# Kernel tuning notes

Hardware: AMD Instinct MI355X
Metric: run time of the kernel (lower is better)

## Reference

```python
import jax, jax.numpy as jnp
import numpy as np

NUM_RELATIONS = 3


def _rgcn(x, W_rel, W_root, bias, src, dst, etype):
    # PyG RGCNConv: out = x @ W_root + bias + sum_r mean_{e: type(e)=r, dst(e)=i} (x_src @ W_r)
    n = x.shape[0]
    xr = jnp.einsum('ni,rio->rno', x, W_rel)          # [R, N, F] relation-transformed nodes
    msg = xr[etype, src]                               # [E, F] per-edge messages
    out = x @ W_root + bias
    for r in range(NUM_RELATIONS):
        m = (etype == r)
        s = jax.ops.segment_sum(jnp.where(m[:, None], msg, 0.0), dst, num_segments=n)
        c = jax.ops.segment_sum(m.astype(x.dtype), dst, num_segments=n)
        out = out + s / jnp.maximum(c, 1.0)[:, None]   # mean aggregation per relation
    return out


def _gate(h, q, Wg, bg, Wq, bq):
    # h: [BN, F], q: [B, L, F]
    B, L, F = q.shape
    N = h.shape[0] // B
    h3 = h.reshape(B, N, F)
    # w_gate(cat([h_i, q_l])) = h_i @ Wg[:, :F].T + q_l @ Wg[:, F:].T + bg
    hg = jnp.einsum('bnf,gf->bng', h3, Wg[:, :F])                    # [B,N,F]
    qg = jnp.einsum('blf,gf->blg', q, Wg[:, F:]) + bg                # [B,L,F]
    attn = jax.nn.sigmoid(hg[:, :, None, :] + qg[:, None, :, :])     # [B,N,L,F]
    qi = jnp.einsum('bnlf,blf->bnf', attn, q)                        # [B,N,F]
    alpha = jax.nn.sigmoid(
        jnp.einsum('bnf,gf->bng', h3, Wq[:, :F])
        + jnp.einsum('bnf,gf->bng', qi, Wq[:, F:]) + bq)
    hn = alpha * jnp.tanh(qi) + (1.0 - alpha) * h3
    return hn.reshape(B * N, F)


def setup_inputs() -> dict:
    key = jax.random.key(0)
    ks = jax.random.split(key, 16)
    F = 768
    BN, E, B, L = 2048, 65536, 8, 64
    s = 0.02
    return {
        'x': jax.random.normal(ks[0], (BN, F), jnp.float32),
        'edge_index': jax.random.randint(ks[1], (2, E), 0, BN),
        'edge_type': jax.random.randint(ks[2], (E,), 0, NUM_RELATIONS),
        'query_embs': jax.random.normal(ks[3], (B, L, F), jnp.float32),
        'W_rel1': jax.random.normal(ks[4], (NUM_RELATIONS, F, F), jnp.float32) * s,
        'W_root1': jax.random.normal(ks[5], (F, F), jnp.float32) * s,
        'b1': jnp.zeros((F,), jnp.float32),
        'W_rel2': jax.random.normal(ks[6], (NUM_RELATIONS, F, F), jnp.float32) * s,
        'W_root2': jax.random.normal(ks[7], (F, F), jnp.float32) * s,
        'b2': jnp.zeros((F,), jnp.float32),
        'Wg': jax.random.normal(ks[8], (F, 2 * F), jnp.float32) * s,
        'bg': jnp.zeros((F,), jnp.float32),
        'Wq': jax.random.normal(ks[9], (F, 2 * F), jnp.float32) * s,
        'bq': jnp.zeros((F,), jnp.float32),
    }


def reference(x, edge_index, edge_type, query_embs,
              W_rel1, W_root1, b1, W_rel2, W_root2, b2, Wg, bg, Wq, bq):
    src, dst = edge_index[0], edge_index[1]
    h = jax.nn.relu(_rgcn(x, W_rel1, W_root1, b1, src, dst, edge_type))
    h = _gate(h, query_embs, Wg, bg, Wq, bq)
    h = jax.nn.relu(_rgcn(h, W_rel2, W_root2, b2, src, dst, edge_type))
    h = _gate(h, query_embs, Wg, bg, Wq, bq)
    return h
```

## Files before the change

kernel.cpp:

```cpp
#include <hip/hip_runtime.h>
#include <hip/hip_bf16.h>
#include <cstdint>
#include <cstddef>

#define F 768

typedef float f32x4 __attribute__((ext_vector_type(4)));
typedef short s16x8 __attribute__((ext_vector_type(8)));
typedef short s16x4 __attribute__((ext_vector_type(4)));

#define NEG_LOG2E (-1.4426950408889634f)

__device__ __forceinline__ float bf2f(unsigned short u) {
  union { unsigned int i; float f; } v; v.i = ((unsigned int)u) << 16; return v.f;
}
__device__ __forceinline__ unsigned short f2bf(float f) {
  union { float f; unsigned int i; } v; v.f = f;
  unsigned int r = v.i + 0x7FFF + ((v.i >> 16) & 1);
  return (unsigned short)(r >> 16);
}

#if __has_builtin(__builtin_amdgcn_exp2f)
__device__ __forceinline__ float fexp2(float x) { return __builtin_amdgcn_exp2f(x); }
#else
__device__ __forceinline__ float fexp2(float x) { return exp2f(x); }
#endif
#if __has_builtin(__builtin_amdgcn_rcpf)
__device__ __forceinline__ float frcp(float x) { return __builtin_amdgcn_rcpf(x); }
#else
__device__ __forceinline__ float frcp(float x) { return 1.0f / x; }
#endif

__device__ __forceinline__ float ftanh(float x) {
  float t = fexp2(x * 2.8853900817779268f);
  float s = frcp(t + 1.0f);
  return fmaf(-2.0f, s, 1.0f);
}

__device__ __forceinline__ void gload16(const void* g, void* l) {
  __builtin_amdgcn_global_load_lds(
      (const __attribute__((address_space(1))) void*)g,
      (__attribute__((address_space(3))) void*)l, 16, 0, 0);
}

__global__ void khist(const int* __restrict__ ei, int E, int* __restrict__ cnt) {
  int e = blockIdx.x * blockDim.x + threadIdx.x;
  if (e < E) atomicAdd(&cnt[ei[E + e]], 1);
}

__global__ void kscan(const int* __restrict__ cnt, int* __restrict__ offs, int n) {
  __shared__ int part[256];
  int t = threadIdx.x;
  const int per = n / 256;
  int local[8];
  int s = 0;
  for (int j = 0; j < per; ++j) { local[j] = cnt[t * per + j]; s += local[j]; }
  part[t] = s;
  __syncthreads();
  for (int d = 1; d < 256; d <<= 1) {
    int v = (t >= d) ? part[t - d] : 0;
    __syncthreads();
    part[t] += v;
    __syncthreads();
  }
  int run = (t == 0) ? 0 : part[t - 1];
  for (int j = 0; j < per; ++j) { offs[t * per + j] = run; run += local[j]; }
  if (t == 255) offs[n] = run;
}

__global__ void kscatter(const int* __restrict__ ei, const int* __restrict__ et, int E,
                         const int* __restrict__ offs, int* __restrict__ cur,
                         int* __restrict__ sorted) {
  int e = blockIdx.x * blockDim.x + threadIdx.x;
  if (e >= E) return;
  int dst = ei[E + e];
  int pos = offs[dst] + atomicAdd(&cur[dst], 1);
  sorted[pos] = ei[e] | (et[e] << 16);
}

__global__ void kcvt(const float* __restrict__ src, int lds_,
                     unsigned short* __restrict__ dst, int ldd) {
  const int r = blockIdx.x, c = threadIdx.x * 4;
  float4 v = *(const float4*)(src + (size_t)r * lds_ + c);
  s16x4 o;
  o[0] = (short)f2bf(v.x); o[1] = (short)f2bf(v.y);
  o[2] = (short)f2bf(v.z); o[3] = (short)f2bf(v.w);
  *(s16x4*)(dst + (size_t)r * ldd + c) = o;
}

__global__ void kcvtw(const float* __restrict__ Wg, const float* __restrict__ Wq,
                      unsigned short* __restrict__ Wgq, unsigned short* __restrict__ WgR,
                      unsigned short* __restrict__ WqR) {
  const int b = blockIdx.x, c = threadIdx.x * 4;
  const float* srow;
  unsigned short* drow;
  int off;
  if (b < 1536) {
    srow = (b < 768) ? Wg + (size_t)b * 1536 : Wq + (size_t)(b - 768) * 1536;
    drow = Wgq + (size_t)b * 768;
    off = 0;
  } else if (b < 2304) {
    srow = Wg + (size_t)(b - 1536) * 1536;
    drow = WgR + (size_t)(b - 1536) * 768;
    off = 768;
  } else {
    srow = Wq + (size_t)(b - 2304) * 1536;
    drow = WqR + (size_t)(b - 2304) * 768;
    off = 768;
  }
  float4 v = *(const float4*)(srow + off + c);
  s16x4 o;
  o[0] = (short)f2bf(v.x); o[1] = (short)f2bf(v.y);
  o[2] = (short)f2bf(v.z); o[3] = (short)f2bf(v.w);
  *(s16x4*)(drow + c) = o;
}

__global__ void ktrans(const float* __restrict__ Wr1, const float* __restrict__ Wl1,
                       const float* __restrict__ Wr2, const float* __restrict__ Wl2,
                       unsigned short* __restrict__ Wcat1, unsigned short* __restrict__ Wcat2) {
  __shared__ float tile[64][65];
  const int z = blockIdx.z, layer = z >> 2, part = z & 3;
  const float* src = (part == 0) ? (layer ? Wr2 : Wr1)
                                 : ((layer ? Wl2 : Wl1) + (size_t)(part - 1) * F * F);
  unsigned short* dst = (layer ? Wcat2 : Wcat1) + part * F;
  const int kt = blockIdx.x * 64, nt = blockIdx.y * 64;
  const int t = threadIdx.x, c = t & 63, r4 = t >> 6;
#pragma unroll
  for (int it = 0; it < 16; ++it) {
    int kk = r4 + it * 4;
    tile[kk][c] = src[(size_t)(kt + kk) * F + nt + c];
  }
  __syncthreads();
#pragma unroll
  for (int it = 0; it < 16; ++it) {
    int rr = r4 + it * 4;
    dst[(size_t)(nt + rr) * 3072 + kt + c] = f2bf(tile[c][rr]);
  }
}

__global__ void kagg(const int* __restrict__ offs, const int* __restrict__ sorted,
                     const unsigned short* __restrict__ hin,
                     unsigned short* __restrict__ dst) {
  const int i = blockIdx.x, t = threadIdx.x;
  const int col = t * 4;
  float a0[4] = {}, a1[4] = {}, a2[4] = {};
  int c0 = 0, c1 = 0, c2 = 0;
  const int beg = offs[i], end = offs[i + 1];
  int e = beg;
  for (; e + 1 < end; e += 2) {
    int p0 = sorted[e], p1 = sorted[e + 1];
    s16x4 w0 = *(const s16x4*)(hin + (size_t)(p0 & 0xFFFF) * 3072 + col);
    s16x4 w1 = *(const s16x4*)(hin + (size_t)(p1 & 0xFFFF) * 3072 + col);
    int r0 = p0 >> 16, r1 = p1 >> 16;
    float v0[4], v1[4];
#pragma unroll
    for (int j = 0; j < 4; ++j) {
      v0[j] = bf2f((unsigned short)w0[j]);
      v1[j] = bf2f((unsigned short)w1[j]);
    }
    if (r0 == 0)      { c0++; for (int j = 0; j < 4; ++j) a0[j] += v0[j]; }
    else if (r0 == 1) { c1++; for (int j = 0; j < 4; ++j) a1[j] += v0[j]; }
    else              { c2++; for (int j = 0; j < 4; ++j) a2[j] += v0[j]; }
    if (r1 == 0)      { c0++; for (int j = 0; j < 4; ++j) a0[j] += v1[j]; }
    else if (r1 == 1) { c1++; for (int j = 0; j < 4; ++j) a1[j] += v1[j]; }
    else              { c2++; for (int j = 0; j < 4; ++j) a2[j] += v1[j]; }
  }
  if (e < end) {
    int p0 = sorted[e];
    s16x4 w0 = *(const s16x4*)(hin + (size_t)(p0 & 0xFFFF) * 3072 + col);
    int r0 = p0 >> 16;
    float v0[4];
#pragma unroll
    for (int j = 0; j < 4; ++j) v0[j] = bf2f((unsigned short)w0[j]);
    if (r0 == 0)      { c0++; for (int j = 0; j < 4; ++j) a0[j] += v0[j]; }
    else if (r0 == 1) { c1++; for (int j = 0; j < 4; ++j) a1[j] += v0[j]; }
    else              { c2++; for (int j = 0; j < 4; ++j) a2[j] += v0[j]; }
  }
  const float i0 = frcp((float)(c0 > 0 ? c0 : 1));
  const float i1 = frcp((float)(c1 > 0 ? c1 : 1));
  const float i2 = frcp((float)(c2 > 0 ? c2 : 1));
  unsigned short* d = dst + (size_t)i * 3072 + col;
  s16x4 o;
#pragma unroll
  for (int j = 0; j < 4; ++j) o[j] = (short)f2bf(a0[j] * i0);
  *(s16x4*)d = o;
#pragma unroll
  for (int j = 0; j < 4; ++j) o[j] = (short)f2bf(a1[j] * i1);
  *(s16x4*)(d + F) = o;
#pragma unroll
  for (int j = 0; j < 4; ++j) o[j] = (short)f2bf(a2[j] * i2);
  *(s16x4*)(d + 2 * F) = o;
}

template <int EPI>
__launch_bounds__(256)
__global__ void kmm(const unsigned short* __restrict__ A, int lda,
                    const unsigned short* __restrict__ B, int ldb,
                    float* __restrict__ C, int ldc, int K,
                    const float* __restrict__ bias,
                    const float* __restrict__ aux1,
                    const unsigned short* __restrict__ aux2,
                    unsigned short* __restrict__ C2, int ldc2, float escale) {
  __shared__ unsigned short Asb[2][64 * 64];
  __shared__ unsigned short Bsb[2][64 * 64];
  const int t = threadIdx.x;
  const int lane = t & 63, wid = t >> 6;
  const int wr = wid >> 1, wc = wid & 1;
  const int bm = blockIdx.x * 64, bn = blockIdx.y * 64;

  const int srow = lane >> 3, schunk = lane & 7;
  const int kxor = ((schunk ^ srow) << 3);
  const int rowA = wid * 16 + srow;
  const unsigned short* Ap = A + (size_t)(bm + rowA) * lda + kxor;
  const unsigned short* Bp = B + (size_t)(bn + rowA) * ldb + kxor;
  const int lbase = wid * 16 * 64;

  const int rA0 = wr * 32 + (lane & 15);
  const int rB0 = wc * 32 + (lane & 15);
  const int l7 = lane & 7, lq = lane >> 4;
  const int s8_0 = (((0 * 4 + lq) ^ l7) << 3);
  const int s8_1 = (((1 * 4 + lq) ^ l7) << 3);

  f32x4 acc[2][2] = {};

  auto stage = [&](int cb, int k0) {
#pragma unroll
    for (int j = 0; j < 2; ++j) {
      gload16(Ap + (size_t)j * 8 * lda + k0, &Asb[cb][lbase + j * 512]);
      gload16(Bp + (size_t)j * 8 * ldb + k0, &Bsb[cb][lbase + j * 512]);
    }
  };

  stage(0, 0);
  __syncthreads();
  int cur = 0;
  for (int k0 = 0; k0 < K; k0 += 64) {
    if (k0 + 64 < K) stage(cur ^ 1, k0 + 64);
    const unsigned short* As = Asb[cur];
    const unsigned short* Bs = Bsb[cur];
#pragma unroll
    for (int ks = 0; ks < 2; ++ks) {
      const int s8 = ks ? s8_1 : s8_0;
      s16x8 af[2], bf[2];
#pragma unroll
      for (int i = 0; i < 2; ++i)
        af[i] = *(const s16x8*)(As + (rA0 + i * 16) * 64 + s8);
#pragma unroll
      for (int n = 0; n < 2; ++n)
        bf[n] = *(const s16x8*)(Bs + (rB0 + n * 16) * 64 + s8);
#pragma unroll
      for (int i = 0; i < 2; ++i)
#pragma unroll
        for (int n = 0; n < 2; ++n)
          acc[i][n] = __builtin_amdgcn_mfma_f32_16x16x32_bf16(af[i], bf[n], acc[i][n], 0, 0, 0);
    }
    __syncthreads();
    cur ^= 1;
  }

#pragma unroll
  for (int i = 0; i < 2; ++i)
#pragma unroll
    for (int n = 0; n < 2; ++n)
#pragma unroll
      for (int j = 0; j < 4; ++j) {
        const int row = bm + wr * 32 + i * 16 + (lane >> 4) * 4 + j;
        const int col = bn + wc * 32 + n * 16 + (lane & 15);
        float v = acc[i][n][j];
        if (EPI == 3 || EPI == 4) {
          float zh = aux1[(size_t)row * 1536 + 768 + col];
          float z = v + bias[col] + zh;
          float al = frcp(1.0f + fexp2(z * NEG_LOG2E));
          float tq = aux1[(size_t)row * 1536 + col];
          float hv = bf2f(aux2[(size_t)row * 768 + col]);
          float o = al * tq + (1.0f - al) * hv;
          if (EPI == 3) C2[(size_t)row * ldc2 + col] = f2bf(o);
          else          C[(size_t)row * ldc + col] = o;
        } else if (EPI == 5) {
          float es = (bn < 768) ? escale : 1.0f;
          C[(size_t)row * ldc + col] = v * es;
        } else if (EPI == 6) {
          C[(size_t)row * ldc + col] = (v + bias[col]) * escale;
        }
      }
}

__launch_bounds__(256)
__global__ void kmm_pk(const unsigned short* __restrict__ A, int lda,
                       const unsigned short* __restrict__ B, int ldb,
                       float* __restrict__ P, int Ksplit, int pstride) {
  __shared__ unsigned short Asb[2][64 * 64];
  __shared__ unsigned short Bsb[2][64 * 64];
  const int t = threadIdx.x;
  const int lane = t & 63, wid = t >> 6;
  const int wr = wid >> 1, wc = wid & 1;
  const int bm = blockIdx.x * 64, bn = blockIdx.y * 64;
  const int kbase = blockIdx.z * Ksplit;
  float* Cp = P + (size_t)blockIdx.z * pstride;

  const int srow = lane >> 3, schunk = lane & 7;
  const int kxor = ((schunk ^ srow) << 3);
  const int rowA = wid * 16 + srow;
  const unsigned short* Ap = A + (size_t)(bm + rowA) * lda + kxor + kbase;
  const unsigned short* Bp = B + (size_t)(bn + rowA) * ldb + kxor + kbase;
  const int lbase = wid * 16 * 64;

  const int rA0 = wr * 32 + (lane & 15);
  const int rB0 = wc * 32 + (lane & 15);
  const int l7 = lane & 7, lq = lane >> 4;
  const int s8_0 = (((0 * 4 + lq) ^ l7) << 3);
  const int s8_1 = (((1 * 4 + lq) ^ l7) << 3);

  f32x4 acc[2][2] = {};

  auto stage = [&](int cb, int k0) {
#pragma unroll
    for (int j = 0; j < 2; ++j) {
      gload16(Ap + (size_t)j * 8 * lda + k0, &Asb[cb][lbase + j * 512]);
      gload16(Bp + (size_t)j * 8 * ldb + k0, &Bsb[cb][lbase + j * 512]);
    }
  };

  stage(0, 0);
  __syncthreads();
  int cur = 0;
  for (int k0 = 0; k0 < Ksplit; k0 += 64) {
    if (k0 + 64 < Ksplit) stage(cur ^ 1, k0 + 64);
    const unsigned short* As = Asb[cur];
    const unsigned short* Bs = Bsb[cur];
#pragma unroll
    for (int ks = 0; ks < 2; ++ks) {
      const int s8 = ks ? s8_1 : s8_0;
      s16x8 af[2], bf[2];
#pragma unroll
      for (int i = 0; i < 2; ++i)
        af[i] = *(const s16x8*)(As + (rA0 + i * 16) * 64 + s8);
#pragma unroll
      for (int n = 0; n < 2; ++n)
        bf[n] = *(const s16x8*)(Bs + (rB0 + n * 16) * 64 + s8);
#pragma unroll
      for (int i = 0; i < 2; ++i)
#pragma unroll
        for (int n = 0; n < 2; ++n)
          acc[i][n] = __builtin_amdgcn_mfma_f32_16x16x32_bf16(af[i], bf[n], acc[i][n], 0, 0, 0);
    }
    __syncthreads();
    cur ^= 1;
  }

#pragma unroll
  for (int i = 0; i < 2; ++i)
#pragma unroll
    for (int n = 0; n < 2; ++n)
#pragma unroll
      for (int j = 0; j < 4; ++j) {
        const int row = bm + wr * 32 + i * 16 + (lane >> 4) * 4 + j;
        const int col = bn + wc * 32 + n * 16 + (lane & 15);
        Cp[(size_t)row * F + col] = acc[i][n][j];
      }
}

__global__ void kep_relu(const float* __restrict__ P, int pstride,
                         const float* __restrict__ bias,
                         unsigned short* __restrict__ hb) {
  const int idx = (blockIdx.x * 256 + threadIdx.x) * 4;
  const int col = idx - (idx / F) * F;
  float4 s = *(const float4*)(P + idx);
  const float4 s1 = *(const float4*)(P + pstride + idx);
  const float4 s2 = *(const float4*)(P + 2 * (size_t)pstride + idx);
  const float4 s3 = *(const float4*)(P + 3 * (size_t)pstride + idx);
  const float4 bv = *(const float4*)(bias + col);
  s.x = fmaxf(s.x + s1.x + s2.x + s3.x + bv.x, 0.0f);
  s.y = fmaxf(s.y + s1.y + s2.y + s3.y + bv.y, 0.0f);
  s.z = fmaxf(s.z + s1.z + s2.z + s3.z + bv.z, 0.0f);
  s.w = fmaxf(s.w + s1.w + s2.w + s3.w + bv.w, 0.0f);
  s16x4 o;
  o[0] = (short)f2bf(s.x); o[1] = (short)f2bf(s.y);
  o[2] = (short)f2bf(s.z); o[3] = (short)f2bf(s.w);
  *(s16x4*)(hb + idx) = o;
}

__global__ void kqi(float* __restrict__ hgz, const float* __restrict__ q,
                    const float* __restrict__ qgp,
                    unsigned short* __restrict__ qib,
                    int npb, int L) {
  const int t = threadIdx.x;
  const int g0 = blockIdx.x * 2;
  const int b = g0 / npb;
  float hgv[2][3], acc[2][3];
#pragma unroll
  for (int nn = 0; nn < 2; ++nn)
#pragma unroll
    for (int c = 0; c < 3; ++c) {
      hgv[nn][c] = hgz[(size_t)(g0 + nn) * 1536 + c * 256 + t];
      acc[nn][c] = 0.0f;
    }
  const float* qb = q + (size_t)b * L * F;
  const float* qgb = qgp + (size_t)b * L * F;
#pragma unroll 4
  for (int l = 0; l < L; ++l) {
    float qr[3], qgr[3];
#pragma unroll
    for (int c = 0; c < 3; ++c) {
      qr[c] = qb[(size_t)l * F + c * 256 + t];
      qgr[c] = qgb[(size_t)l * F + c * 256 + t];
    }
#pragma unroll
    for (int nn = 0; nn < 2; ++nn)
#pragma unroll
      for (int c = 0; c < 3; ++c) {
        float s = frcp(1.0f + fexp2(hgv[nn][c] + qgr[c]));
        acc[nn][c] = fmaf(s, qr[c], acc[nn][c]);
      }
  }
#pragma unroll
  for (int nn = 0; nn < 2; ++nn)
#pragma unroll
    for (int c = 0; c < 3; ++c) {
      const int g = g0 + nn, cc = c * 256 + t;
      qib[(size_t)g * F + cc] = f2bf(acc[nn][c]);
      hgz[(size_t)g * 1536 + cc] = ftanh(acc[nn][c]);
    }
}

extern "C" void kernel_launch(void* const* d_in, const int* in_sizes, int n_in,
                              void* d_out, int out_size, void* d_ws, size_t ws_size,
                              hipStream_t stream) {
  const float* x = (const float*)d_in[0];
  const int* ei = (const int*)d_in[1];
  const int* et = (const int*)d_in[2];
  const float* q = (const float*)d_in[3];
  const float* Wrel1 = (const float*)d_in[4];
  const float* Wroot1 = (const float*)d_in[5];
  const float* b1 = (const float*)d_in[6];
  const float* Wrel2 = (const float*)d_in[7];
  const float* Wroot2 = (const float*)d_in[8];
  const float* b2 = (const float*)d_in[9];
  const float* Wg = (const float*)d_in[10];
  const float* bg = (const float*)d_in[11];
  const float* Wq = (const float*)d_in[12];
  const float* bq = (const float*)d_in[13];

  const int BNn = in_sizes[0] / F;
  const int E = in_sizes[1] / 2;
  const int L = 64;
  const int Bq = in_sizes[3] / (L * F);
  const int npb = BNn / Bq;
  const int ML = Bq * L;
  const int PSTR = BNn * F;
  float* out = (float*)d_out;

  char* p = (char*)d_ws;
  auto alloc = [&](size_t bytes) {
    void* r = (void*)p;
    p += (bytes + 255) & ~(size_t)255;
    return r;
  };
  int* cnt = (int*)alloc((size_t)BNn * 4);
  int* cur = (int*)alloc((size_t)BNn * 4);
  int* offs = (int*)alloc((size_t)(BNn + 1) * 4);
  int* sorted = (int*)alloc((size_t)E * 4);
  unsigned short* Acat = (unsigned short*)alloc((size_t)BNn * 3072 * 2);
  unsigned short* Wcat1 = (unsigned short*)alloc((size_t)F * 3072 * 2);
  unsigned short* Wcat2 = (unsigned short*)alloc((size_t)F * 3072 * 2);
  unsigned short* Wgq = (unsigned short*)alloc((size_t)1536 * F * 2);
  unsigned short* WgR = (unsigned short*)alloc((size_t)F * F * 2);
  unsigned short* WqR = (unsigned short*)alloc((size_t)F * F * 2);
  unsigned short* qbf = (unsigned short*)alloc((size_t)ML * F * 2);
  float* qg = (float*)alloc((size_t)ML * F * 4);
  unsigned short* hb = (unsigned short*)alloc((size_t)BNn * F * 2);
  float* hgz = (float*)alloc((size_t)BNn * 1536 * 4);
  unsigned short* qib = (unsigned short*)alloc((size_t)BNn * F * 2);
  float* parts = (float*)alloc((size_t)4 * PSTR * 4);

  hipMemsetAsync(cnt, 0, (size_t)BNn * 4, stream);
  hipMemsetAsync(cur, 0, (size_t)BNn * 4, stream);
  khist<<<(E + 255) / 256, 256, 0, stream>>>(ei, E, cnt);
  kscan<<<1, 256, 0, stream>>>(cnt, offs, BNn);
  kscatter<<<(E + 255) / 256, 256, 0, stream>>>(ei, et, E, offs, cur, sorted);

  kcvt<<<BNn, 192, 0, stream>>>(x, F, Acat, 3072);
  kcvt<<<ML, 192, 0, stream>>>(q, F, qbf, F);
  kcvtw<<<3072, 192, 0, stream>>>(Wg, Wq, Wgq, WgR, WqR);
  ktrans<<<dim3(12, 12, 8), 256, 0, stream>>>(Wroot1, Wrel1, Wroot2, Wrel2, Wcat1, Wcat2);

  kmm<6><<<dim3(ML / 64, F / 64), 256, 0, stream>>>(
      qbf, F, WgR, F, qg, F, F, bg, nullptr, nullptr, nullptr, 0, NEG_LOG2E);

  for (int layer = 0; layer < 2; ++layer) {
    const unsigned short* Wcat = layer ? Wcat2 : Wcat1;
    const float* bb = layer ? b2 : b1;

    kagg<<<BNn, 192, 0, stream>>>(offs, sorted, Acat, Acat + F);

    kmm_pk<<<dim3(BNn / 64, F / 64, 4), 256, 0, stream>>>(
        Acat, 3072, Wcat, 3072, parts, F, PSTR);

    kep_relu<<<(BNn * F) / 1024, 256, 0, stream>>>(parts, PSTR, bb, hb);

    kmm<5><<<dim3(BNn / 64, 1536 / 64), 256, 0, stream>>>(
        hb, F, Wgq, F, hgz, 1536, F, nullptr, nullptr, nullptr, nullptr, 0, NEG_LOG2E);

    kqi<<<BNn / 2, 256, 0, stream>>>(hgz, q, qg, qib, npb, L);

    if (layer == 0) {
      kmm<3><<<dim3(BNn / 64, F / 64), 256, 0, stream>>>(
          qib, F, WqR, F, nullptr, 0, F, bq, hgz, hb, Acat, 3072, 0.f);
    } else {
      kmm<4><<<dim3(BNn / 64, F / 64), 256, 0, stream>>>(
          qib, F, WqR, F, out, F, F, bq, hgz, hb, nullptr, 0, 0.f);
    }
  }
}
```

Before: 338.1 us.

## Fuse gate attention reduction into GEMM epilogue and merge small launches

Removes the separate kqi kernel by computing the sigmoid-weighted sum over query tokens in a new GEMM epilogue (EPI 7). It works directly on the accumulator tiles for the first 768 output columns, which avoids writing and rereading the hg half of hgz. It also merges the two conversion launches and the two memsets into one each, and unrolls the edge aggregation loop by four to issue more gathers in flight. The cost is that the epilogue does 64 iterations of exp and reciprocal per element inside the GEMM blocks, which can add register pressure and load imbalance because only half the column blocks do this work.

After: 335.0 us. About the same (-0.9%).

```diff
diff --git a/kernel.cpp b/kernel.cpp
--- a/kernel.cpp
+++ b/kernel.cpp
@@ -78,14 +78,18 @@
   sorted[pos] = ei[e] | (et[e] << 16);
 }
 
-__global__ void kcvt(const float* __restrict__ src, int lds_,
-                     unsigned short* __restrict__ dst, int ldd) {
+__global__ void kcvt(const float* __restrict__ x, const float* __restrict__ q, int nx,
+                     unsigned short* __restrict__ Acat, unsigned short* __restrict__ qbf) {
   const int r = blockIdx.x, c = threadIdx.x * 4;
-  float4 v = *(const float4*)(src + (size_t)r * lds_ + c);
+  const float* srow;
+  unsigned short* drow;
+  if (r < nx) { srow = x + (size_t)r * F; drow = Acat + (size_t)r * 3072; }
+  else        { srow = q + (size_t)(r - nx) * F; drow = qbf + (size_t)(r - nx) * F; }
+  float4 v = *(const float4*)(srow + c);
   s16x4 o;
   o[0] = (short)f2bf(v.x); o[1] = (short)f2bf(v.y);
   o[2] = (short)f2bf(v.z); o[3] = (short)f2bf(v.w);
-  *(s16x4*)(dst + (size_t)r * ldd + c) = o;
+  *(s16x4*)(drow + c) = o;
 }
 
 __global__ void kcvtw(const float* __restrict__ Wg, const float* __restrict__ Wq,
@@ -147,25 +151,26 @@
   int c0 = 0, c1 = 0, c2 = 0;
   const int beg = offs[i], end = offs[i + 1];
   int e = beg;
-  for (; e + 1 < end; e += 2) {
-    int p0 = sorted[e], p1 = sorted[e + 1];
-    s16x4 w0 = *(const s16x4*)(hin + (size_t)(p0 & 0xFFFF) * 3072 + col);
-    s16x4 w1 = *(const s16x4*)(hin + (size_t)(p1 & 0xFFFF) * 3072 + col);
-    int r0 = p0 >> 16, r1 = p1 >> 16;
-    float v0[4], v1[4];
-#pragma unroll
-    for (int j = 0; j < 4; ++j) {
-      v0[j] = bf2f((unsigned short)w0[j]);
-      v1[j] = bf2f((unsigned short)w1[j]);
-    }
-    if (r0 == 0)      { c0++; for (int j = 0; j < 4; ++j) a0[j] += v0[j]; }
-    else if (r0 == 1) { c1++; for (int j = 0; j < 4; ++j) a1[j] += v0[j]; }
-    else              { c2++; for (int j = 0; j < 4; ++j) a2[j] += v0[j]; }
-    if (r1 == 0)      { c0++; for (int j = 0; j < 4; ++j) a0[j] += v1[j]; }
-    else if (r1 == 1) { c1++; for (int j = 0; j < 4; ++j) a1[j] += v1[j]; }
-    else              { c2++; for (int j = 0; j < 4; ++j) a2[j] += v1[j]; }
-  }
-  if (e < end) {
+  for (; e + 3 < end; e += 4) {
+    int pk[4];
+#pragma unroll
+    for (int u = 0; u < 4; ++u) pk[u] = sorted[e + u];
+    s16x4 w[4];
+#pragma unroll
+    for (int u = 0; u < 4; ++u)
+      w[u] = *(const s16x4*)(hin + (size_t)(pk[u] & 0xFFFF) * 3072 + col);
+#pragma unroll
+    for (int u = 0; u < 4; ++u) {
+      int r = pk[u] >> 16;
+      float v[4];
+#pragma unroll
+      for (int j = 0; j < 4; ++j) v[j] = bf2f((unsigned short)w[u][j]);
+      if (r == 0)      { c0++; for (int j = 0; j < 4; ++j) a0[j] += v[j]; }
+      else if (r == 1) { c1++; for (int j = 0; j < 4; ++j) a1[j] += v[j]; }
+      else             { c2++; for (int j = 0; j < 4; ++j) a2[j] += v[j]; }
+    }
+  }
+  for (; e < end; ++e) {
     int p0 = sorted[e];
     s16x4 w0 = *(const s16x4*)(hin + (size_t)(p0 & 0xFFFF) * 3072 + col);
     int r0 = p0 >> 16;
@@ -200,7 +205,8 @@
                     const float* __restrict__ bias,
                     const float* __restrict__ aux1,
                     const unsigned short* __restrict__ aux2,
-                    unsigned short* __restrict__ C2, int ldc2, float escale) {
+                    unsigned short* __restrict__ C2, int ldc2,
+                    float escale, int Lq) {
   __shared__ unsigned short Asb[2][64 * 64];
   __shared__ unsigned short Bsb[2][64 * 64];
   const int t = threadIdx.x;
@@ -256,6 +262,49 @@
     }
     __syncthreads();
     cur ^= 1;
+  }
+
+  if (EPI == 7 && bn < 768) {
+    float hgp[2][2][4], qacc[2][2][4];
+#pragma unroll
+    for (int i = 0; i < 2; ++i)
+#pragma unroll
+      for (int n = 0; n < 2; ++n)
+#pragma unroll
+        for (int j = 0; j < 4; ++j) {
+          hgp[i][n][j] = acc[i][n][j] * NEG_LOG2E;
+          qacc[i][n][j] = 0.0f;
+        }
+    const int b = bm >> 8;
+    const int col0 = bn + wc * 32 + (lane & 15);
+    const float* qb = aux1 + (size_t)b * Lq * F;
+    const float* qgb = bias + (size_t)b * Lq * F;
+#pragma unroll 2
+    for (int l = 0; l < Lq; ++l) {
+      const float qg0 = qgb[(size_t)l * F + col0];
+      const float qg1 = qgb[(size_t)l * F + col0 + 16];
+      const float q0 = qb[(size_t)l * F + col0];
+      const float q1 = qb[(size_t)l * F + col0 + 16];
+#pragma unroll
+      for (int i = 0; i < 2; ++i)
+#pragma unroll
+        for (int j = 0; j < 4; ++j) {
+          qacc[i][0][j] = fmaf(frcp(1.0f + fexp2(hgp[i][0][j] + qg0)), q0, qacc[i][0][j]);
+          qacc[i][1][j] = fmaf(frcp(1.0f + fexp2(hgp[i][1][j] + qg1)), q1, qacc[i][1][j]);
+        }
+    }
+#pragma unroll
+    for (int i = 0; i < 2; ++i)
+#pragma unroll
+      for (int n = 0; n < 2; ++n)
+#pragma unroll
+        for (int j = 0; j < 4; ++j) {
+          const int row = bm + wr * 32 + i * 16 + (lane >> 4) * 4 + j;
+          const int col = col0 + n * 16;
+          C2[(size_t)row * 768 + col] = f2bf(qacc[i][n][j]);
+          C[(size_t)row * 1536 + col] = ftanh(qacc[i][n][j]);
+        }
+    return;
   }
 
 #pragma unroll
@@ -276,11 +325,10 @@
           float o = al * tq + (1.0f - al) * hv;
           if (EPI == 3) C2[(size_t)row * ldc2 + col] = f2bf(o);
           else          C[(size_t)row * ldc + col] = o;
-        } else if (EPI == 5) {
-          float es = (bn < 768) ? escale : 1.0f;
-          C[(size_t)row * ldc + col] = v * es;
         } else if (EPI == 6) {
           C[(size_t)row * ldc + col] = (v + bias[col]) * escale;
+        } else {
+          C[(size_t)row * ldc + col] = v;
         }
       }
 }
@@ -380,49 +428,6 @@
   *(s16x4*)(hb + idx) = o;
 }
 
-__global__ void kqi(float* __restrict__ hgz, const float* __restrict__ q,
-                    const float* __restrict__ qgp,
-                    unsigned short* __restrict__ qib,
-                    int npb, int L) {
-  const int t = threadIdx.x;
-  const int g0 = blockIdx.x * 2;
-  const int b = g0 / npb;
-  float hgv[2][3], acc[2][3];
-#pragma unroll
-  for (int nn = 0; nn < 2; ++nn)
-#pragma unroll
-    for (int c = 0; c < 3; ++c) {
-      hgv[nn][c] = hgz[(size_t)(g0 + nn) * 1536 + c * 256 + t];
-      acc[nn][c] = 0.0f;
-    }
-  const float* qb = q + (size_t)b * L * F;
-  const float* qgb = qgp + (size_t)b * L * F;
-#pragma unroll 4
-  for (int l = 0; l < L; ++l) {
-    float qr[3], qgr[3];
-#pragma unroll
-    for (int c = 0; c < 3; ++c) {
-      qr[c] = qb[(size_t)l * F + c * 256 + t];
-      qgr[c] = qgb[(size_t)l * F + c * 256 + t];
-    }
-#pragma unroll
-    for (int nn = 0; nn < 2; ++nn)
-#pragma unroll
-      for (int c = 0; c < 3; ++c) {
-        float s = frcp(1.0f + fexp2(hgv[nn][c] + qgr[c]));
-        acc[nn][c] = fmaf(s, qr[c], acc[nn][c]);
-      }
-  }
-#pragma unroll
-  for (int nn = 0; nn < 2; ++nn)
-#pragma unroll
-    for (int c = 0; c < 3; ++c) {
-      const int g = g0 + nn, cc = c * 256 + t;
-      qib[(size_t)g * F + cc] = f2bf(acc[nn][c]);
-      hgz[(size_t)g * 1536 + cc] = ftanh(acc[nn][c]);
-    }
-}
-
 extern "C" void kernel_launch(void* const* d_in, const int* in_sizes, int n_in,
                               void* d_out, int out_size, void* d_ws, size_t ws_size,
                               hipStream_t stream) {
@@ -445,7 +450,6 @@
   const int E = in_sizes[1] / 2;
   const int L = 64;
   const int Bq = in_sizes[3] / (L * F);
-  const int npb = BNn / Bq;
   const int ML = Bq * L;
   const int PSTR = BNn * F;
   float* out = (float*)d_out;
@@ -456,8 +460,9 @@
     p += (bytes + 255) & ~(size_t)255;
     return r;
   };
-  int* cnt = (int*)alloc((size_t)BNn * 4);
-  int* cur = (int*)alloc((size_t)BNn * 4);
+  int* cntcur = (int*)alloc((size_t)2 * BNn * 4);
+  int* cnt = cntcur;
+  int* cur = cntcur + BNn;
   int* offs = (int*)alloc((size_t)(BNn + 1) * 4);
   int* sorted = (int*)alloc((size_t)E * 4);
   unsigned short* Acat = (unsigned short*)alloc((size_t)BNn * 3072 * 2);
@@ -473,19 +478,17 @@
   unsigned short* qib = (unsigned short*)alloc((size_t)BNn * F * 2);
   float* parts = (float*)alloc((size_t)4 * PSTR * 4);
 
-  hipMemsetAsync(cnt, 0, (size_t)BNn * 4, stream);
-  hipMemsetAsync(cur, 0, (size_t)BNn * 4, stream);
+  hipMemsetAsync(cntcur, 0, (size_t)2 * BNn * 4, stream);
   khist<<<(E + 255) / 256, 256, 0, stream>>>(ei, E, cnt);
   kscan<<<1, 256, 0, stream>>>(cnt, offs, BNn);
   kscatter<<<(E + 255) / 256, 256, 0, stream>>>(ei, et, E, offs, cur, sorted);
 
-  kcvt<<<BNn, 192, 0, stream>>>(x, F, Acat, 3072);
-  kcvt<<<ML, 192, 0, stream>>>(q, F, qbf, F);
+  kcvt<<<BNn + ML, 192, 0, stream>>>(x, q, BNn, Acat, qbf);
   kcvtw<<<3072, 192, 0, stream>>>(Wg, Wq, Wgq, WgR, WqR);
   ktrans<<<dim3(12, 12, 8), 256, 0, stream>>>(Wroot1, Wrel1, Wroot2, Wrel2, Wcat1, Wcat2);
 
   kmm<6><<<dim3(ML / 64, F / 64), 256, 0, stream>>>(
-      qbf, F, WgR, F, qg, F, F, bg, nullptr, nullptr, nullptr, 0, NEG_LOG2E);
+      qbf, F, WgR, F, qg, F, F, bg, nullptr, nullptr, nullptr, 0, NEG_LOG2E, L);
 
   for (int layer = 0; layer < 2; ++layer) {
     const unsigned short* Wcat = layer ? Wcat2 : Wcat1;
@@ -498,17 +501,15 @@
 
     kep_relu<<<(BNn * F) / 1024, 256, 0, stream>>>(parts, PSTR, bb, hb);
 
-    kmm<5><<<dim3(BNn / 64, 1536 / 64), 256, 0, stream>>>(
-        hb, F, Wgq, F, hgz, 1536, F, nullptr, nullptr, nullptr, nullptr, 0, NEG_LOG2E);
-
-    kqi<<<BNn / 2, 256, 0, stream>>>(hgz, q, qg, qib, npb, L);
+    kmm<7><<<dim3(BNn / 64, 1536 / 64), 256, 0, stream>>>(
+        hb, F, Wgq, F, hgz, 1536, F, qg, q, nullptr, qib, F, 0.f, L);
 
     if (layer == 0) {
       kmm<3><<<dim3(BNn / 64, F / 64), 256, 0, stream>>>(
-          qib, F, WqR, F, nullptr, 0, F, bq, hgz, hb, Acat, 3072, 0.f);
+          qib, F, WqR, F, nullptr, 0, F, bq, hgz, hb, Acat, 3072, 0.f, L);
     } else {
       kmm<4><<<dim3(BNn / 64, F / 64), 256, 0, stream>>>(
-          qib, F, WqR, F, out, F, F, bq, hgz, hb, nullptr, 0, 0.f);
-    }
-  }
-}
+          qib, F, WqR, F, out, F, F, bq, hgz, hb, nullptr, 0, 0.f, L);
+    }
+  }
+}
```
